# Performance work log

Measured on AMD Instinct MI355X. Metric: run time of the kernel, lower is better.

## Reference

```python
import jax, jax.numpy as jnp
import numpy as np

N_NODES = 100000
N_EDGES = 1600000
IN_DIM, HID_DIM, OUT_DIM = 128, 64, 40


def setup_inputs() -> dict:
    key = jax.random.key(0)
    k1, k2, k3, k4, k5, k6 = jax.random.split(key, 6)
    x = jax.random.normal(k1, (N_NODES, IN_DIM), dtype=jnp.float32)
    edge_index = jax.random.randint(k2, (2, N_EDGES), 0, N_NODES, dtype=jnp.int64)
    W1 = jax.random.normal(k3, (IN_DIM, HID_DIM), dtype=jnp.float32) * 0.05
    b1 = jnp.zeros((HID_DIM,), dtype=jnp.float32)
    W2 = jax.random.normal(k4, (HID_DIM, OUT_DIM), dtype=jnp.float32) * 0.05
    b2 = jnp.zeros((OUT_DIM,), dtype=jnp.float32)
    return {"x": x, "edge_index": edge_index, "W1": W1, "b1": b1, "W2": W2, "b2": b2}


def gcn_conv(x, src, dst, W, b, n_nodes):
    """PyG GCNConv: linear -> symmetric-normalized aggregation (with self loops) -> + bias."""
    h = x @ W                                                # [N, C_out]
    # degree of targets, including the implicit self loop (weight 1 each)
    deg = jax.ops.segment_sum(jnp.ones_like(dst, dtype=h.dtype), dst,
                              num_segments=n_nodes) + 1.0    # [N]
    dinv = jax.lax.rsqrt(deg)                                # deg >= 1, always valid
    norm = dinv[src] * dinv[dst]                             # [E] edge norm coefficients
    msg = h[src] * norm[:, None]                             # [E, C_out] gather + scale
    agg = jax.ops.segment_sum(msg, dst, num_segments=n_nodes)
    # self-loop contribution: norm_ii = dinv_i * dinv_i
    agg = agg + h * (dinv * dinv)[:, None]
    return agg + b


def reference(x, edge_index, W1, b1, W2, b2):
    src, dst = edge_index[0], edge_index[1]  # source_to_target flow (PyG default)
    n = x.shape[0]
    h = gcn_conv(x, src, dst, W1, b1, n)
    h = jax.nn.relu(h)
    # dropout is identity in eval mode (training=False)
    out = gcn_conv(h, src, dst, W2, b2, n)
    return out
```

## Files before the change

kernel.cpp:

```cpp
#include <hip/hip_runtime.h>
#include <math.h>

#define N_NODES 100000
#define N_EDGES 1600000
#define IN_DIM 128
#define HID_DIM 64
#define OUT_DIM 40

#define NPAD 102400

#define BUCKET_SHIFT 7
#define BUCKET_NODES 128
#define N_BUCKETS 782
#define CHUNK 2048
#define N_CHUNKS 784

typedef _Float16 f16;
typedef _Float16 f16x2 __attribute__((ext_vector_type(2)));
typedef _Float16 f16x4 __attribute__((ext_vector_type(4)));
typedef _Float16 f16x8 __attribute__((ext_vector_type(8)));
typedef float f32x4 __attribute__((ext_vector_type(4)));


__global__ __launch_bounds__(256) void hist_kernel(const int* __restrict__ dst,
                                                   int* __restrict__ hist) {
    __shared__ int lh[N_BUCKETS];
    int c = blockIdx.x;
    int t = threadIdx.x;
    for (int b = t; b < N_BUCKETS; b += 256) lh[b] = 0;
    __syncthreads();
    int e0 = c * CHUNK;
    for (int i = t; i < CHUNK; i += 256) {
        int e = e0 + i;
        if (e < N_EDGES) atomicAdd(&lh[dst[e] >> BUCKET_SHIFT], 1);
    }
    __syncthreads();
    for (int b = t; b < N_BUCKETS; b += 256) hist[c * N_BUCKETS + b] = lh[b];
}

__global__ __launch_bounds__(256) void scan_chunks_kernel(const int* __restrict__ hist,
                                                          int* __restrict__ base,
                                                          int* __restrict__ bucketTotal) {
    __shared__ int lds[256];
    int b = blockIdx.x;
    int t = threadIdx.x;
    int v[4];
    int s = 0;
    for (int k = 0; k < 4; ++k) {
        int c = 4 * t + k;
        int cv = (c < N_CHUNKS) ? hist[c * N_BUCKETS + b] : 0;
        v[k] = s;
        s += cv;
    }
    lds[t] = s;
    __syncthreads();
    for (int off = 1; off < 256; off <<= 1) {
        int val = (t >= off) ? lds[t - off] : 0;
        __syncthreads();
        lds[t] += val;
        __syncthreads();
    }
    int excl = (t == 0) ? 0 : lds[t - 1];
    for (int k = 0; k < 4; ++k) {
        int c = 4 * t + k;
        if (c < N_CHUNKS) base[b * N_CHUNKS + c] = excl + v[k];
    }
    if (t == 255) bucketTotal[b] = lds[255];
}

__global__ __launch_bounds__(256) void scan_buckets_kernel(const int* __restrict__ bucketTotal,
                                                           int* __restrict__ bucketBase) {
    __shared__ int lds[256];
    int t = threadIdx.x;
    int v[4];
    int s = 0;
    for (int k = 0; k < 4; ++k) {
        int b = 4 * t + k;
        int cv = (b < N_BUCKETS) ? bucketTotal[b] : 0;
        v[k] = s;
        s += cv;
    }
    lds[t] = s;
    __syncthreads();
    for (int off = 1; off < 256; off <<= 1) {
        int val = (t >= off) ? lds[t - off] : 0;
        __syncthreads();
        lds[t] += val;
        __syncthreads();
    }
    int excl = (t == 0) ? 0 : lds[t - 1];
    for (int k = 0; k < 4; ++k) {
        int b = 4 * t + k;
        if (b < N_BUCKETS) bucketBase[b] = excl + v[k];
    }
}

__global__ __launch_bounds__(256) void scatter_kernel(const int* __restrict__ src,
                                                      const int* __restrict__ dst,
                                                      const int* __restrict__ base,
                                                      const int* __restrict__ bucketBase,
                                                      int* __restrict__ stage) {
    __shared__ int lbase[N_BUCKETS];
    __shared__ int lcnt[N_BUCKETS];
    int bid = blockIdx.x;
    int chunk = (bid & 7) * 98 + (bid >> 3);
    int t = threadIdx.x;
    for (int b = t; b < N_BUCKETS; b += 256) {
        lbase[b] = base[b * N_CHUNKS + chunk] + bucketBase[b];
        lcnt[b] = 0;
    }
    __syncthreads();
    int e0 = chunk * CHUNK;
    for (int i = t; i < CHUNK; i += 256) {
        int e = e0 + i;
        if (e < N_EDGES) {
            int d = dst[e];
            int b = d >> BUCKET_SHIFT;
            int pos = lbase[b] + atomicAdd(&lcnt[b], 1);
            stage[pos] = ((d & (BUCKET_NODES - 1)) << 17) | src[e];
        }
    }
}

__global__ __launch_bounds__(256) void place_kernel(const int* __restrict__ stage,
                                                    const int* __restrict__ bucketBase,
                                                    int* __restrict__ csr,
                                                    int* __restrict__ row_start,
                                                    int* __restrict__ cnt,
                                                    float* __restrict__ dinv) {
    __shared__ int lhist[BUCKET_NODES];
    __shared__ int lscan[BUCKET_NODES];
    __shared__ int lstart[BUCKET_NODES];
    __shared__ int lcur[BUCKET_NODES];
    int b = blockIdx.x;
    int t = threadIdx.x;
    int est = bucketBase[b];
    int een = (b == N_BUCKETS - 1) ? N_EDGES : bucketBase[b + 1];
    if (t < BUCKET_NODES) { lhist[t] = 0; lcur[t] = 0; }
    __syncthreads();
    for (int e = est + t; e < een; e += 256) atomicAdd(&lhist[stage[e] >> 17], 1);
    __syncthreads();
    if (t < BUCKET_NODES) lscan[t] = lhist[t];
    __syncthreads();
    for (int off = 1; off < BUCKET_NODES; off <<= 1) {
        int val = (t >= off && t < BUCKET_NODES) ? lscan[t - off] : 0;
        __syncthreads();
        if (t < BUCKET_NODES) lscan[t] += val;
        __syncthreads();
    }
    if (t < BUCKET_NODES) {
        int myexcl = (t == 0) ? 0 : lscan[t - 1];
        lstart[t] = est + myexcl;
        int node = (b << BUCKET_SHIFT) + t;
        if (node < N_NODES) {
            row_start[node] = est + myexcl;
            cnt[node] = lhist[t];
            dinv[node] = rsqrtf((float)lhist[t] + 1.0f);
        }
    }
    __syncthreads();
    for (int e = est + t; e < een; e += 256) {
        int rec = stage[e];
        int dl = rec >> 17;
        int pos = lstart[dl] + atomicAdd(&lcur[dl], 1);
        csr[pos] = rec & 0x1FFFF;
    }
}

__global__ __launch_bounds__(256) void wfrag_kernel(const float* __restrict__ W1,
                                                    const float* __restrict__ W2,
                                                    f16* __restrict__ w1f,
                                                    f16* __restrict__ w2f) {
    int g = blockIdx.x * 256 + threadIdx.x;
    if (g < 1024) {
        int f = g >> 6, L = g & 63;
        int s = f >> 2, c = f & 3;
        int q = L >> 4, n = L & 15;
        f16x8 v;
#pragma unroll
        for (int j = 0; j < 8; ++j) v[j] = (f16)W1[(32 * s + 8 * q + j) * HID_DIM + 16 * c + n];
        *(f16x8*)&w1f[(size_t)g * 8] = v;
    } else if (g < 1024 + 384) {
        int gg = g - 1024;
        int f = gg >> 6, L = gg & 63;
        int s = f / 3, c = f % 3;
        int q = L >> 4, n = L & 15;
        int col = 16 * c + n;
        f16x8 v;
#pragma unroll
        for (int j = 0; j < 8; ++j)
            v[j] = (col < OUT_DIM) ? (f16)W2[(32 * s + 8 * q + j) * OUT_DIM + col] : (f16)0.f;
        *(f16x8*)&w2f[(size_t)gg * 8] = v;
    }
}

__global__ __launch_bounds__(256) void gemm1_kernel(const float* __restrict__ x,
                                                    const f16* __restrict__ w1f,
                                                    const float* __restrict__ dinv,
                                                    f16* __restrict__ h1p) {
    __shared__ f16 aT[1088 * 8];
    int t = threadIdx.x;
    int nodeBase = blockIdx.x * 64;
    int L = t & 63;

    const f16x8* w1f8 = (const f16x8*)w1f;
    f16x8 bfrag[16];
#pragma unroll
    for (int f = 0; f < 16; ++f) bfrag[f] = w1f8[f * 64 + L];

#pragma unroll
    for (int i = 0; i < 8; ++i) {
        int idx = i * 256 + t;
        int node = idx >> 5;
        int col4 = idx & 31;
        int gnode = nodeBase + node;
        if (gnode >= N_NODES) gnode = N_NODES - 1;
        float4 v = *(const float4*)&x[(size_t)gnode * IN_DIM + col4 * 4];
        int w = node >> 4, m = node & 15;
        int s = col4 >> 3, q = (col4 >> 1) & 3, j0 = (col4 & 1) * 4;
        f16x4 h;
        h.x = (f16)v.x; h.y = (f16)v.y; h.z = (f16)v.z; h.w = (f16)v.w;
        int idx16 = (w * 4 + s) * 68 + 17 * q + m;
        *(f16x4*)&aT[idx16 * 8 + j0] = h;
    }
    __syncthreads();

    int wv = t >> 6;
    int q = L >> 4, m = L & 15;
    f32x4 acc[4] = {};
#pragma unroll
    for (int s = 0; s < 4; ++s) {
        f16x8 afrag = *(const f16x8*)&aT[((wv * 4 + s) * 68 + 17 * q + m) * 8];
#pragma unroll
        for (int c = 0; c < 4; ++c)
            acc[c] = __builtin_amdgcn_mfma_f32_16x16x32_f16(afrag, bfrag[s * 4 + c], acc[c], 0, 0, 0);
    }

#pragma unroll
    for (int r = 0; r < 4; ++r) {
        int node = nodeBase + 16 * wv + q * 4 + r;
        if (node < N_NODES) {
            float di = dinv[node];
#pragma unroll
            for (int c = 0; c < 4; ++c)
                h1p[(size_t)node * HID_DIM + 16 * c + m] = (f16)(acc[c][r] * di);
        }
    }
}

#define ZSTR 72
__global__ __launch_bounds__(256) void agg1mm_kernel(const f16* __restrict__ h1p,
                                                     const int* __restrict__ csr,
                                                     const int* __restrict__ row_start,
                                                     const int* __restrict__ cnt,
                                                     const float* __restrict__ dinv,
                                                     const float* __restrict__ b1,
                                                     const f16* __restrict__ w2f,
                                                     f16* __restrict__ h2p) {
    __shared__ f16 zT[64 * ZSTR];
    int t = threadIdx.x;
    int nodeBase = blockIdx.x * 64;
    int wv = t >> 6;
    int L = t & 63;
    int g = L >> 3;
    int s = L & 7;
    const f16x8* h8 = (const f16x8*)h1p;
    float bb[8];
#pragma unroll
    for (int j = 0; j < 8; ++j) bb[j] = b1[8 * s + j];

    for (int p = 0; p < 2; ++p) {
        int nodeLocal = 16 * wv + 8 * p + g;
        int node = nodeBase + nodeLocal;
        float acc[8];
#pragma unroll
        for (int j = 0; j < 8; ++j) acc[j] = 0.f;
        int lim = 0;
        const int* cp = csr;
        bool valid = (node < N_NODES);
        if (valid) {
            f16x8 sv = h8[(size_t)node * 8 + s];
#pragma unroll
            for (int j = 0; j < 8; ++j) acc[j] = (float)sv[j];
            lim = cnt[node];
            cp = csr + row_start[node];
        }
        for (int k = 0; k < lim; k += 4) {
            int k1 = (k + 1 < lim) ? k + 1 : k;
            int k2 = (k + 2 < lim) ? k + 2 : k;
            int k3 = (k + 3 < lim) ? k + 3 : k;
            int i0 = cp[k], i1 = cp[k1], i2 = cp[k2], i3 = cp[k3];
            f16x8 f0 = h8[(size_t)i0 * 8 + s];
            f16x8 f1 = h8[(size_t)i1 * 8 + s];
            f16x8 f2 = h8[(size_t)i2 * 8 + s];
            f16x8 f3 = h8[(size_t)i3 * 8 + s];
            float m1 = (k + 1 < lim) ? 1.f : 0.f;
            float m2 = (k + 2 < lim) ? 1.f : 0.f;
            float m3 = (k + 3 < lim) ? 1.f : 0.f;
#pragma unroll
            for (int j = 0; j < 8; ++j)
                acc[j] += (float)f0[j] + m1 * (float)f1[j] + m2 * (float)f2[j] + m3 * (float)f3[j];
        }
        f16x8 o;
        if (valid) {
            float di = dinv[node];
#pragma unroll
            for (int j = 0; j < 8; ++j) {
                float v = acc[j] * di + bb[j];
                o[j] = (f16)(v > 0.f ? v : 0.f);
            }
        } else {
#pragma unroll
            for (int j = 0; j < 8; ++j) o[j] = (f16)0.f;
        }
        *(f16x8*)&zT[nodeLocal * ZSTR + 8 * s] = o;
    }
    __syncthreads();

    int q = L >> 4, m = L & 15;
    const f16x8* w2f8 = (const f16x8*)w2f;
    f32x4 acc2[3] = {};
#pragma unroll
    for (int ks = 0; ks < 2; ++ks) {
        f16x8 afrag = *(const f16x8*)&zT[(16 * wv + m) * ZSTR + 32 * ks + 8 * q];
#pragma unroll
        for (int c = 0; c < 3; ++c)
            acc2[c] = __builtin_amdgcn_mfma_f32_16x16x32_f16(afrag, w2f8[(ks * 3 + c) * 64 + L], acc2[c], 0, 0, 0);
    }
#pragma unroll
    for (int r = 0; r < 4; ++r) {
        int node = nodeBase + 16 * wv + q * 4 + r;
        if (node < N_NODES) {
            float di = dinv[node];
            h2p[(size_t)node * OUT_DIM + m]      = (f16)(acc2[0][r] * di);
            h2p[(size_t)node * OUT_DIM + 16 + m] = (f16)(acc2[1][r] * di);
            if (m < 8)
                h2p[(size_t)node * OUT_DIM + 32 + m] = (f16)(acc2[2][r] * di);
        }
    }
}

__global__ __launch_bounds__(256) void agg2_kernel(const f16* __restrict__ h2p,
                                                   const int* __restrict__ csr,
                                                   const int* __restrict__ row_start,
                                                   const int* __restrict__ cnt,
                                                   const float* __restrict__ dinv,
                                                   const float* __restrict__ b2,
                                                   float* __restrict__ out) {
    int t = threadIdx.x;
    int node = blockIdx.x * 32 + (t >> 3);
    int s = t & 7;
    if (node >= N_NODES || s >= 5) return;
    const f16x8* h8 = (const f16x8*)h2p;
    float acc[8];
    {
        f16x8 sv = h8[(size_t)node * 5 + s];
#pragma unroll
        for (int j = 0; j < 8; ++j) acc[j] = (float)sv[j];
    }
    int lim = cnt[node];
    const int* cp = csr + row_start[node];
    for (int k = 0; k < lim; k += 4) {
        int k1 = (k + 1 < lim) ? k + 1 : k;
        int k2 = (k + 2 < lim) ? k + 2 : k;
        int k3 = (k + 3 < lim) ? k + 3 : k;
        int i0 = cp[k], i1 = cp[k1], i2 = cp[k2], i3 = cp[k3];
        f16x8 f0 = h8[(size_t)i0 * 5 + s];
        f16x8 f1 = h8[(size_t)i1 * 5 + s];
        f16x8 f2 = h8[(size_t)i2 * 5 + s];
        f16x8 f3 = h8[(size_t)i3 * 5 + s];
        float m1 = (k + 1 < lim) ? 1.f : 0.f;
        float m2 = (k + 2 < lim) ? 1.f : 0.f;
        float m3 = (k + 3 < lim) ? 1.f : 0.f;
#pragma unroll
        for (int j = 0; j < 8; ++j)
            acc[j] += (float)f0[j] + m1 * (float)f1[j] + m2 * (float)f2[j] + m3 * (float)f3[j];
    }
    float di = dinv[node];
    float4 o0, o1;
    o0.x = acc[0] * di + b2[8 * s + 0];
    o0.y = acc[1] * di + b2[8 * s + 1];
    o0.z = acc[2] * di + b2[8 * s + 2];
    o0.w = acc[3] * di + b2[8 * s + 3];
    o1.x = acc[4] * di + b2[8 * s + 4];
    o1.y = acc[5] * di + b2[8 * s + 5];
    o1.z = acc[6] * di + b2[8 * s + 6];
    o1.w = acc[7] * di + b2[8 * s + 7];
    *(float4*)&out[(size_t)node * OUT_DIM + 8 * s] = o0;
    *(float4*)&out[(size_t)node * OUT_DIM + 8 * s + 4] = o1;
}

extern "C" void kernel_launch(void* const* d_in, const int* in_sizes, int n_in,
                              void* d_out, int out_size, void* d_ws, size_t ws_size,
                              hipStream_t stream) {
    const float* x  = (const float*)d_in[0];
    const int*   ei = (const int*)d_in[1];
    const float* W1 = (const float*)d_in[2];
    const float* b1 = (const float*)d_in[3];
    const float* W2 = (const float*)d_in[4];
    const float* b2 = (const float*)d_in[5];
    float* out = (float*)d_out;

    const int* src = ei;
    const int* dst = ei + N_EDGES;

    int* wsi        = (int*)d_ws;
    int* hist       = wsi;
    int* base       = hist + N_CHUNKS * N_BUCKETS;
    int* bucketTotal= base + N_BUCKETS * N_CHUNKS;
    int* bucketBase = bucketTotal + 1024;
    int* row_start  = bucketBase + 1024;
    int* cnt        = row_start + NPAD;
    int* csr        = cnt + NPAD;
    int* stage      = csr + N_EDGES;
    float* dinv     = (float*)(stage + N_EDGES);
    f16*   h1p      = (f16*)(dinv + NPAD);
    f16*   h2p      = h1p + (size_t)N_NODES * HID_DIM;
    f16*   w1f      = h2p + (size_t)N_NODES * OUT_DIM;
    f16*   w2f      = w1f + 8192;

    hist_kernel<<<N_CHUNKS, 256, 0, stream>>>(dst, hist);
    scan_chunks_kernel<<<N_BUCKETS, 256, 0, stream>>>(hist, base, bucketTotal);
    scan_buckets_kernel<<<1, 256, 0, stream>>>(bucketTotal, bucketBase);
    scatter_kernel<<<N_CHUNKS, 256, 0, stream>>>(src, dst, base, bucketBase, stage);
    place_kernel<<<N_BUCKETS, 256, 0, stream>>>(stage, bucketBase, csr, row_start, cnt, dinv);

    wfrag_kernel<<<6, 256, 0, stream>>>(W1, W2, w1f, w2f);
    gemm1_kernel<<<(N_NODES + 63) / 64, 256, 0, stream>>>(x, w1f, dinv, h1p);
    agg1mm_kernel<<<(N_NODES + 63) / 64, 256, 0, stream>>>(h1p, csr, row_start, cnt, dinv, b1, w2f, h2p);
    agg2_kernel<<<(N_NODES + 31) / 32, 256, 0, stream>>>(h2p, csr, row_start, cnt, dinv, b2, out);
}
```

Before: 217.3 us.

## Fuse all GCN stages into one persistent cooperative kernel with grid syncs

Replaces the nine separate launches (histogram, scans, scatter, place, weight fragmenting, gemm1, agg1+mm, agg2) with a single cooperative persistent kernel. Each stage loops over its work items with a grid-stride loop and the stages are separated by grid.sync(). This targets per-launch overhead and inter-kernel gaps. In exchange it adds grid-wide barrier cost, caps occupancy at the cooperative grid size, and forces all stages to share one register and shared-memory footprint.

```diff
diff --git a/kernel.cpp b/kernel.cpp
--- a/kernel.cpp
+++ b/kernel.cpp
@@ -1,5 +1,8 @@
 #include <hip/hip_runtime.h>
+#include <hip/hip_cooperative_groups.h>
 #include <math.h>
+
+namespace cg = cooperative_groups;
 
 #define N_NODES 100000
 #define N_EDGES 1600000
@@ -15,379 +18,394 @@
 #define CHUNK 2048
 #define N_CHUNKS 784
 
+#define G1_TILES 1563
+#define AGG2_TILES 3125
+
 typedef _Float16 f16;
 typedef _Float16 f16x2 __attribute__((ext_vector_type(2)));
 typedef _Float16 f16x4 __attribute__((ext_vector_type(4)));
 typedef _Float16 f16x8 __attribute__((ext_vector_type(8)));
 typedef float f32x4 __attribute__((ext_vector_type(4)));
 
-
-__global__ __launch_bounds__(256) void hist_kernel(const int* __restrict__ dst,
-                                                   int* __restrict__ hist) {
-    __shared__ int lh[N_BUCKETS];
-    int c = blockIdx.x;
+#define ZSTR 72
+
+__global__ __launch_bounds__(256) void gcn_mega_kernel(
+    const float* __restrict__ x, const int* __restrict__ ei,
+    const float* __restrict__ W1, const float* __restrict__ b1,
+    const float* __restrict__ W2, const float* __restrict__ b2,
+    float* __restrict__ out, int* __restrict__ wsi)
+{
+    int* hist        = wsi;
+    int* base        = hist + N_CHUNKS * N_BUCKETS;
+    int* bucketTotal = base + N_BUCKETS * N_CHUNKS;
+    int* bucketBase  = bucketTotal + 1024;
+    int* row_start   = bucketBase + 1024;
+    int* cnt         = row_start + NPAD;
+    int* csr         = cnt + NPAD;
+    int* stage       = csr + N_EDGES;
+    float* dinv      = (float*)(stage + N_EDGES);
+    f16* h1p         = (f16*)(dinv + NPAD);
+    f16* h2p         = h1p + (size_t)N_NODES * HID_DIM;
+    f16* w1f         = h2p + (size_t)N_NODES * OUT_DIM;
+    f16* w2f         = w1f + 8192;
+    const int* src = ei;
+    const int* dst = ei + N_EDGES;
+
+    cg::grid_group grid = cg::this_grid();
+    __shared__ alignas(16) unsigned char smemraw[17408];
     int t = threadIdx.x;
-    for (int b = t; b < N_BUCKETS; b += 256) lh[b] = 0;
-    __syncthreads();
-    int e0 = c * CHUNK;
-    for (int i = t; i < CHUNK; i += 256) {
-        int e = e0 + i;
-        if (e < N_EDGES) atomicAdd(&lh[dst[e] >> BUCKET_SHIFT], 1);
-    }
-    __syncthreads();
-    for (int b = t; b < N_BUCKETS; b += 256) hist[c * N_BUCKETS + b] = lh[b];
-}
-
-__global__ __launch_bounds__(256) void scan_chunks_kernel(const int* __restrict__ hist,
-                                                          int* __restrict__ base,
-                                                          int* __restrict__ bucketTotal) {
-    __shared__ int lds[256];
-    int b = blockIdx.x;
-    int t = threadIdx.x;
-    int v[4];
-    int s = 0;
-    for (int k = 0; k < 4; ++k) {
-        int c = 4 * t + k;
-        int cv = (c < N_CHUNKS) ? hist[c * N_BUCKETS + b] : 0;
-        v[k] = s;
-        s += cv;
-    }
-    lds[t] = s;
-    __syncthreads();
-    for (int off = 1; off < 256; off <<= 1) {
-        int val = (t >= off) ? lds[t - off] : 0;
+    int G = gridDim.x;
+
+    {
+        int* lh = (int*)smemraw;
+        for (int c = blockIdx.x; c < N_CHUNKS; c += G) {
+            for (int b = t; b < N_BUCKETS; b += 256) lh[b] = 0;
+            __syncthreads();
+            int e0 = c * CHUNK;
+            for (int i = t; i < CHUNK; i += 256) {
+                int e = e0 + i;
+                if (e < N_EDGES) atomicAdd(&lh[dst[e] >> BUCKET_SHIFT], 1);
+            }
+            __syncthreads();
+            for (int b = t; b < N_BUCKETS; b += 256) hist[c * N_BUCKETS + b] = lh[b];
+            __syncthreads();
+        }
+    }
+    grid.sync();
+
+    {
+        int* lds = (int*)smemraw;
+        for (int b = blockIdx.x; b < N_BUCKETS; b += G) {
+            int v[4];
+            int s = 0;
+            for (int k = 0; k < 4; ++k) {
+                int c = 4 * t + k;
+                int cv = (c < N_CHUNKS) ? hist[c * N_BUCKETS + b] : 0;
+                v[k] = s;
+                s += cv;
+            }
+            lds[t] = s;
+            __syncthreads();
+            for (int off = 1; off < 256; off <<= 1) {
+                int val = (t >= off) ? lds[t - off] : 0;
+                __syncthreads();
+                lds[t] += val;
+                __syncthreads();
+            }
+            int excl = (t == 0) ? 0 : lds[t - 1];
+            for (int k = 0; k < 4; ++k) {
+                int c = 4 * t + k;
+                if (c < N_CHUNKS) base[b * N_CHUNKS + c] = excl + v[k];
+            }
+            if (t == 255) bucketTotal[b] = lds[255];
+            __syncthreads();
+        }
+    }
+    grid.sync();
+
+    if (blockIdx.x == 0) {
+        int* lds = (int*)smemraw;
+        int v[4];
+        int s = 0;
+        for (int k = 0; k < 4; ++k) {
+            int b = 4 * t + k;
+            int cv = (b < N_BUCKETS) ? bucketTotal[b] : 0;
+            v[k] = s;
+            s += cv;
+        }
+        lds[t] = s;
         __syncthreads();
-        lds[t] += val;
-        __syncthreads();
-    }
-    int excl = (t == 0) ? 0 : lds[t - 1];
-    for (int k = 0; k < 4; ++k) {
-        int c = 4 * t + k;
-        if (c < N_CHUNKS) base[b * N_CHUNKS + c] = excl + v[k];
-    }
-    if (t == 255) bucketTotal[b] = lds[255];
-}
-
-__global__ __launch_bounds__(256) void scan_buckets_kernel(const int* __restrict__ bucketTotal,
-                                                           int* __restrict__ bucketBase) {
-    __shared__ int lds[256];
-    int t = threadIdx.x;
-    int v[4];
-    int s = 0;
-    for (int k = 0; k < 4; ++k) {
-        int b = 4 * t + k;
-        int cv = (b < N_BUCKETS) ? bucketTotal[b] : 0;
-        v[k] = s;
-        s += cv;
-    }
-    lds[t] = s;
-    __syncthreads();
-    for (int off = 1; off < 256; off <<= 1) {
-        int val = (t >= off) ? lds[t - off] : 0;
-        __syncthreads();
-        lds[t] += val;
-        __syncthreads();
-    }
-    int excl = (t == 0) ? 0 : lds[t - 1];
-    for (int k = 0; k < 4; ++k) {
-        int b = 4 * t + k;
-        if (b < N_BUCKETS) bucketBase[b] = excl + v[k];
-    }
-}
-
-__global__ __launch_bounds__(256) void scatter_kernel(const int* __restrict__ src,
-                                                      const int* __restrict__ dst,
-                                                      const int* __restrict__ base,
-                                                      const int* __restrict__ bucketBase,
-                                                      int* __restrict__ stage) {
-    __shared__ int lbase[N_BUCKETS];
-    __shared__ int lcnt[N_BUCKETS];
-    int bid = blockIdx.x;
-    int chunk = (bid & 7) * 98 + (bid >> 3);
-    int t = threadIdx.x;
-    for (int b = t; b < N_BUCKETS; b += 256) {
-        lbase[b] = base[b * N_CHUNKS + chunk] + bucketBase[b];
-        lcnt[b] = 0;
-    }
-    __syncthreads();
-    int e0 = chunk * CHUNK;
-    for (int i = t; i < CHUNK; i += 256) {
-        int e = e0 + i;
-        if (e < N_EDGES) {
-            int d = dst[e];
-            int b = d >> BUCKET_SHIFT;
-            int pos = lbase[b] + atomicAdd(&lcnt[b], 1);
-            stage[pos] = ((d & (BUCKET_NODES - 1)) << 17) | src[e];
-        }
-    }
-}
-
-__global__ __launch_bounds__(256) void place_kernel(const int* __restrict__ stage,
-                                                    const int* __restrict__ bucketBase,
-                                                    int* __restrict__ csr,
-                                                    int* __restrict__ row_start,
-                                                    int* __restrict__ cnt,
-                                                    float* __restrict__ dinv) {
-    __shared__ int lhist[BUCKET_NODES];
-    __shared__ int lscan[BUCKET_NODES];
-    __shared__ int lstart[BUCKET_NODES];
-    __shared__ int lcur[BUCKET_NODES];
-    int b = blockIdx.x;
-    int t = threadIdx.x;
-    int est = bucketBase[b];
-    int een = (b == N_BUCKETS - 1) ? N_EDGES : bucketBase[b + 1];
-    if (t < BUCKET_NODES) { lhist[t] = 0; lcur[t] = 0; }
-    __syncthreads();
-    for (int e = est + t; e < een; e += 256) atomicAdd(&lhist[stage[e] >> 17], 1);
-    __syncthreads();
-    if (t < BUCKET_NODES) lscan[t] = lhist[t];
-    __syncthreads();
-    for (int off = 1; off < BUCKET_NODES; off <<= 1) {
-        int val = (t >= off && t < BUCKET_NODES) ? lscan[t - off] : 0;
-        __syncthreads();
-        if (t < BUCKET_NODES) lscan[t] += val;
-        __syncthreads();
-    }
-    if (t < BUCKET_NODES) {
-        int myexcl = (t == 0) ? 0 : lscan[t - 1];
-        lstart[t] = est + myexcl;
-        int node = (b << BUCKET_SHIFT) + t;
-        if (node < N_NODES) {
-            row_start[node] = est + myexcl;
-            cnt[node] = lhist[t];
-            dinv[node] = rsqrtf((float)lhist[t] + 1.0f);
-        }
-    }
-    __syncthreads();
-    for (int e = est + t; e < een; e += 256) {
-        int rec = stage[e];
-        int dl = rec >> 17;
-        int pos = lstart[dl] + atomicAdd(&lcur[dl], 1);
-        csr[pos] = rec & 0x1FFFF;
-    }
-}
-
-__global__ __launch_bounds__(256) void wfrag_kernel(const float* __restrict__ W1,
-                                                    const float* __restrict__ W2,
-                                                    f16* __restrict__ w1f,
-                                                    f16* __restrict__ w2f) {
-    int g = blockIdx.x * 256 + threadIdx.x;
-    if (g < 1024) {
-        int f = g >> 6, L = g & 63;
-        int s = f >> 2, c = f & 3;
-        int q = L >> 4, n = L & 15;
-        f16x8 v;
-#pragma unroll
-        for (int j = 0; j < 8; ++j) v[j] = (f16)W1[(32 * s + 8 * q + j) * HID_DIM + 16 * c + n];
-        *(f16x8*)&w1f[(size_t)g * 8] = v;
-    } else if (g < 1024 + 384) {
-        int gg = g - 1024;
-        int f = gg >> 6, L = gg & 63;
-        int s = f / 3, c = f % 3;
-        int q = L >> 4, n = L & 15;
-        int col = 16 * c + n;
-        f16x8 v;
-#pragma unroll
-        for (int j = 0; j < 8; ++j)
-            v[j] = (col < OUT_DIM) ? (f16)W2[(32 * s + 8 * q + j) * OUT_DIM + col] : (f16)0.f;
-        *(f16x8*)&w2f[(size_t)gg * 8] = v;
-    }
-}
-
-__global__ __launch_bounds__(256) void gemm1_kernel(const float* __restrict__ x,
-                                                    const f16* __restrict__ w1f,
-                                                    const float* __restrict__ dinv,
-                                                    f16* __restrict__ h1p) {
-    __shared__ f16 aT[1088 * 8];
-    int t = threadIdx.x;
-    int nodeBase = blockIdx.x * 64;
-    int L = t & 63;
-
-    const f16x8* w1f8 = (const f16x8*)w1f;
-    f16x8 bfrag[16];
-#pragma unroll
-    for (int f = 0; f < 16; ++f) bfrag[f] = w1f8[f * 64 + L];
-
-#pragma unroll
-    for (int i = 0; i < 8; ++i) {
-        int idx = i * 256 + t;
-        int node = idx >> 5;
-        int col4 = idx & 31;
-        int gnode = nodeBase + node;
-        if (gnode >= N_NODES) gnode = N_NODES - 1;
-        float4 v = *(const float4*)&x[(size_t)gnode * IN_DIM + col4 * 4];
-        int w = node >> 4, m = node & 15;
-        int s = col4 >> 3, q = (col4 >> 1) & 3, j0 = (col4 & 1) * 4;
-        f16x4 h;
-        h.x = (f16)v.x; h.y = (f16)v.y; h.z = (f16)v.z; h.w = (f16)v.w;
-        int idx16 = (w * 4 + s) * 68 + 17 * q + m;
-        *(f16x4*)&aT[idx16 * 8 + j0] = h;
-    }
-    __syncthreads();
-
-    int wv = t >> 6;
-    int q = L >> 4, m = L & 15;
-    f32x4 acc[4] = {};
-#pragma unroll
-    for (int s = 0; s < 4; ++s) {
-        f16x8 afrag = *(const f16x8*)&aT[((wv * 4 + s) * 68 + 17 * q + m) * 8];
-#pragma unroll
-        for (int c = 0; c < 4; ++c)
-            acc[c] = __builtin_amdgcn_mfma_f32_16x16x32_f16(afrag, bfrag[s * 4 + c], acc[c], 0, 0, 0);
-    }
-
-#pragma unroll
-    for (int r = 0; r < 4; ++r) {
-        int node = nodeBase + 16 * wv + q * 4 + r;
-        if (node < N_NODES) {
-            float di = dinv[node];
-#pragma unroll
-            for (int c = 0; c < 4; ++c)
-                h1p[(size_t)node * HID_DIM + 16 * c + m] = (f16)(acc[c][r] * di);
-        }
-    }
-}
-
-#define ZSTR 72
-__global__ __launch_bounds__(256) void agg1mm_kernel(const f16* __restrict__ h1p,
-                                                     const int* __restrict__ csr,
-                                                     const int* __restrict__ row_start,
-                                                     const int* __restrict__ cnt,
-                                                     const float* __restrict__ dinv,
-                                                     const float* __restrict__ b1,
-                                                     const f16* __restrict__ w2f,
-                                                     f16* __restrict__ h2p) {
-    __shared__ f16 zT[64 * ZSTR];
-    int t = threadIdx.x;
-    int nodeBase = blockIdx.x * 64;
-    int wv = t >> 6;
-    int L = t & 63;
-    int g = L >> 3;
-    int s = L & 7;
-    const f16x8* h8 = (const f16x8*)h1p;
-    float bb[8];
-#pragma unroll
-    for (int j = 0; j < 8; ++j) bb[j] = b1[8 * s + j];
-
-    for (int p = 0; p < 2; ++p) {
-        int nodeLocal = 16 * wv + 8 * p + g;
-        int node = nodeBase + nodeLocal;
-        float acc[8];
-#pragma unroll
-        for (int j = 0; j < 8; ++j) acc[j] = 0.f;
-        int lim = 0;
-        const int* cp = csr;
-        bool valid = (node < N_NODES);
-        if (valid) {
-            f16x8 sv = h8[(size_t)node * 8 + s];
-#pragma unroll
-            for (int j = 0; j < 8; ++j) acc[j] = (float)sv[j];
-            lim = cnt[node];
-            cp = csr + row_start[node];
-        }
-        for (int k = 0; k < lim; k += 4) {
-            int k1 = (k + 1 < lim) ? k + 1 : k;
-            int k2 = (k + 2 < lim) ? k + 2 : k;
-            int k3 = (k + 3 < lim) ? k + 3 : k;
-            int i0 = cp[k], i1 = cp[k1], i2 = cp[k2], i3 = cp[k3];
-            f16x8 f0 = h8[(size_t)i0 * 8 + s];
-            f16x8 f1 = h8[(size_t)i1 * 8 + s];
-            f16x8 f2 = h8[(size_t)i2 * 8 + s];
-            f16x8 f3 = h8[(size_t)i3 * 8 + s];
-            float m1 = (k + 1 < lim) ? 1.f : 0.f;
-            float m2 = (k + 2 < lim) ? 1.f : 0.f;
-            float m3 = (k + 3 < lim) ? 1.f : 0.f;
-#pragma unroll
-            for (int j = 0; j < 8; ++j)
-                acc[j] += (float)f0[j] + m1 * (float)f1[j] + m2 * (float)f2[j] + m3 * (float)f3[j];
-        }
-        f16x8 o;
-        if (valid) {
-            float di = dinv[node];
-#pragma unroll
-            for (int j = 0; j < 8; ++j) {
-                float v = acc[j] * di + bb[j];
-                o[j] = (f16)(v > 0.f ? v : 0.f);
-            }
-        } else {
-#pragma unroll
-            for (int j = 0; j < 8; ++j) o[j] = (f16)0.f;
-        }
-        *(f16x8*)&zT[nodeLocal * ZSTR + 8 * s] = o;
-    }
-    __syncthreads();
-
-    int q = L >> 4, m = L & 15;
-    const f16x8* w2f8 = (const f16x8*)w2f;
-    f32x4 acc2[3] = {};
-#pragma unroll
-    for (int ks = 0; ks < 2; ++ks) {
-        f16x8 afrag = *(const f16x8*)&zT[(16 * wv + m) * ZSTR + 32 * ks + 8 * q];
-#pragma unroll
-        for (int c = 0; c < 3; ++c)
-            acc2[c] = __builtin_amdgcn_mfma_f32_16x16x32_f16(afrag, w2f8[(ks * 3 + c) * 64 + L], acc2[c], 0, 0, 0);
-    }
-#pragma unroll
-    for (int r = 0; r < 4; ++r) {
-        int node = nodeBase + 16 * wv + q * 4 + r;
-        if (node < N_NODES) {
-            float di = dinv[node];
-            h2p[(size_t)node * OUT_DIM + m]      = (f16)(acc2[0][r] * di);
-            h2p[(size_t)node * OUT_DIM + 16 + m] = (f16)(acc2[1][r] * di);
-            if (m < 8)
-                h2p[(size_t)node * OUT_DIM + 32 + m] = (f16)(acc2[2][r] * di);
-        }
-    }
-}
-
-__global__ __launch_bounds__(256) void agg2_kernel(const f16* __restrict__ h2p,
-                                                   const int* __restrict__ csr,
-                                                   const int* __restrict__ row_start,
-                                                   const int* __restrict__ cnt,
-                                                   const float* __restrict__ dinv,
-                                                   const float* __restrict__ b2,
-                                                   float* __restrict__ out) {
-    int t = threadIdx.x;
-    int node = blockIdx.x * 32 + (t >> 3);
-    int s = t & 7;
-    if (node >= N_NODES || s >= 5) return;
-    const f16x8* h8 = (const f16x8*)h2p;
-    float acc[8];
-    {
-        f16x8 sv = h8[(size_t)node * 5 + s];
-#pragma unroll
-        for (int j = 0; j < 8; ++j) acc[j] = (float)sv[j];
-    }
-    int lim = cnt[node];
-    const int* cp = csr + row_start[node];
-    for (int k = 0; k < lim; k += 4) {
-        int k1 = (k + 1 < lim) ? k + 1 : k;
-        int k2 = (k + 2 < lim) ? k + 2 : k;
-        int k3 = (k + 3 < lim) ? k + 3 : k;
-        int i0 = cp[k], i1 = cp[k1], i2 = cp[k2], i3 = cp[k3];
-        f16x8 f0 = h8[(size_t)i0 * 5 + s];
-        f16x8 f1 = h8[(size_t)i1 * 5 + s];
-        f16x8 f2 = h8[(size_t)i2 * 5 + s];
-        f16x8 f3 = h8[(size_t)i3 * 5 + s];
-        float m1 = (k + 1 < lim) ? 1.f : 0.f;
-        float m2 = (k + 2 < lim) ? 1.f : 0.f;
-        float m3 = (k + 3 < lim) ? 1.f : 0.f;
-#pragma unroll
-        for (int j = 0; j < 8; ++j)
-            acc[j] += (float)f0[j] + m1 * (float)f1[j] + m2 * (float)f2[j] + m3 * (float)f3[j];
-    }
-    float di = dinv[node];
-    float4 o0, o1;
-    o0.x = acc[0] * di + b2[8 * s + 0];
-    o0.y = acc[1] * di + b2[8 * s + 1];
-    o0.z = acc[2] * di + b2[8 * s + 2];
-    o0.w = acc[3] * di + b2[8 * s + 3];
-    o1.x = acc[4] * di + b2[8 * s + 4];
-    o1.y = acc[5] * di + b2[8 * s + 5];
-    o1.z = acc[6] * di + b2[8 * s + 6];
-    o1.w = acc[7] * di + b2[8 * s + 7];
-    *(float4*)&out[(size_t)node * OUT_DIM + 8 * s] = o0;
-    *(float4*)&out[(size_t)node * OUT_DIM + 8 * s + 4] = o1;
+        for (int off = 1; off < 256; off <<= 1) {
+            int val = (t >= off) ? lds[t - off] : 0;
+            __syncthreads();
+            lds[t] += val;
+            __syncthreads();
+        }
+        int excl = (t == 0) ? 0 : lds[t - 1];
+        for (int k = 0; k < 4; ++k) {
+            int b = 4 * t + k;
+            if (b < N_BUCKETS) bucketBase[b] = excl + v[k];
+        }
+    }
+    grid.sync();
+
+    {
+        int* lbase = (int*)smemraw;
+        int* lcnt  = lbase + N_BUCKETS;
+        for (int job = blockIdx.x; job < N_CHUNKS; job += G) {
+            int chunk = (job & 7) * 98 + (job >> 3);
+            for (int b = t; b < N_BUCKETS; b += 256) {
+                lbase[b] = base[b * N_CHUNKS + chunk] + bucketBase[b];
+                lcnt[b] = 0;
+            }
+            __syncthreads();
+            int e0 = chunk * CHUNK;
+            for (int i = t; i < CHUNK; i += 256) {
+                int e = e0 + i;
+                if (e < N_EDGES) {
+                    int d = dst[e];
+                    int b = d >> BUCKET_SHIFT;
+                    int pos = lbase[b] + atomicAdd(&lcnt[b], 1);
+                    stage[pos] = ((d & (BUCKET_NODES - 1)) << 17) | src[e];
+                }
+            }
+            __syncthreads();
+        }
+    }
+    grid.sync();
+
+    {
+        int* lhist  = (int*)smemraw;
+        int* lscan  = lhist + BUCKET_NODES;
+        int* lstart = lscan + BUCKET_NODES;
+        int* lcur   = lstart + BUCKET_NODES;
+        for (int job = blockIdx.x; job < N_BUCKETS + 2; job += G) {
+            if (job < N_BUCKETS) {
+                int b = job;
+                int est = bucketBase[b];
+                int een = (b == N_BUCKETS - 1) ? N_EDGES : bucketBase[b + 1];
+                if (t < BUCKET_NODES) { lhist[t] = 0; lcur[t] = 0; }
+                __syncthreads();
+                for (int e = est + t; e < een; e += 256) atomicAdd(&lhist[stage[e] >> 17], 1);
+                __syncthreads();
+                if (t < BUCKET_NODES) lscan[t] = lhist[t];
+                __syncthreads();
+                for (int off = 1; off < BUCKET_NODES; off <<= 1) {
+                    int val = (t >= off && t < BUCKET_NODES) ? lscan[t - off] : 0;
+                    __syncthreads();
+                    if (t < BUCKET_NODES) lscan[t] += val;
+                    __syncthreads();
+                }
+                if (t < BUCKET_NODES) {
+                    int myexcl = (t == 0) ? 0 : lscan[t - 1];
+                    lstart[t] = est + myexcl;
+                    int node = (b << BUCKET_SHIFT) + t;
+                    if (node < N_NODES) {
+                        row_start[node] = est + myexcl;
+                        cnt[node] = lhist[t];
+                        dinv[node] = rsqrtf((float)lhist[t] + 1.0f);
+                    }
+                }
+                __syncthreads();
+                for (int e = est + t; e < een; e += 256) {
+                    int rec = stage[e];
+                    int dl = rec >> 17;
+                    int pos = lstart[dl] + atomicAdd(&lcur[dl], 1);
+                    csr[pos] = rec & 0x1FFFF;
+                }
+                __syncthreads();
+            } else if (job == N_BUCKETS) {
+                for (int g2 = t; g2 < 1024; g2 += 256) {
+                    int f = g2 >> 6, L = g2 & 63;
+                    int s = f >> 2, c = f & 3;
+                    int q = L >> 4, n = L & 15;
+                    f16x8 v;
+#pragma unroll
+                    for (int j = 0; j < 8; ++j)
+                        v[j] = (f16)W1[(32 * s + 8 * q + j) * HID_DIM + 16 * c + n];
+                    *(f16x8*)&w1f[(size_t)g2 * 8] = v;
+                }
+            } else {
+                for (int g2 = t; g2 < 384; g2 += 256) {
+                    int f = g2 >> 6, L = g2 & 63;
+                    int s = f / 3, c = f % 3;
+                    int q = L >> 4, n = L & 15;
+                    int col = 16 * c + n;
+                    f16x8 v;
+#pragma unroll
+                    for (int j = 0; j < 8; ++j)
+                        v[j] = (col < OUT_DIM) ? (f16)W2[(32 * s + 8 * q + j) * OUT_DIM + col] : (f16)0.f;
+                    *(f16x8*)&w2f[(size_t)g2 * 8] = v;
+                }
+            }
+        }
+    }
+    grid.sync();
+
+    {
+        f16* aT = (f16*)smemraw;
+        int L = t & 63;
+        const f16x8* w1f8 = (const f16x8*)w1f;
+        f16x8 bfrag[16];
+#pragma unroll
+        for (int f = 0; f < 16; ++f) bfrag[f] = w1f8[f * 64 + L];
+
+        for (int job = blockIdx.x; job < G1_TILES; job += G) {
+            int nodeBase = job * 64;
+#pragma unroll
+            for (int i = 0; i < 8; ++i) {
+                int idx = i * 256 + t;
+                int node = idx >> 5;
+                int col4 = idx & 31;
+                int gnode = nodeBase + node;
+                if (gnode >= N_NODES) gnode = N_NODES - 1;
+                float4 v = *(const float4*)&x[(size_t)gnode * IN_DIM + col4 * 4];
+                int w = node >> 4, m = node & 15;
+                int s = col4 >> 3, q = (col4 >> 1) & 3, j0 = (col4 & 1) * 4;
+                f16x4 h;
+                h.x = (f16)v.x; h.y = (f16)v.y; h.z = (f16)v.z; h.w = (f16)v.w;
+                int idx16 = (w * 4 + s) * 68 + 17 * q + m;
+                *(f16x4*)&aT[idx16 * 8 + j0] = h;
+            }
+            __syncthreads();
+
+            int wv = t >> 6;
+            int q = L >> 4, m = L & 15;
+            f32x4 acc[4] = {};
+#pragma unroll
+            for (int s = 0; s < 4; ++s) {
+                f16x8 afrag = *(const f16x8*)&aT[((wv * 4 + s) * 68 + 17 * q + m) * 8];
+#pragma unroll
+                for (int c = 0; c < 4; ++c)
+                    acc[c] = __builtin_amdgcn_mfma_f32_16x16x32_f16(afrag, bfrag[s * 4 + c], acc[c], 0, 0, 0);
+            }
+#pragma unroll
+            for (int r = 0; r < 4; ++r) {
+                int node = nodeBase + 16 * wv + q * 4 + r;
+                if (node < N_NODES) {
+                    float di = dinv[node];
+#pragma unroll
+                    for (int c = 0; c < 4; ++c)
+                        h1p[(size_t)node * HID_DIM + 16 * c + m] = (f16)(acc[c][r] * di);
+                }
+            }
+            __syncthreads();
+        }
+    }
+    grid.sync();
+
+    {
+        f16* zT = (f16*)smemraw;
+        int wv = t >> 6;
+        int L = t & 63;
+        int g = L >> 3;
+        int s = L & 7;
+        const f16x8* h8 = (const f16x8*)h1p;
+        float bb[8];
+#pragma unroll
+        for (int j = 0; j < 8; ++j) bb[j] = b1[8 * s + j];
+        const f16x8* w2f8 = (const f16x8*)w2f;
+
+        for (int job = blockIdx.x; job < G1_TILES; job += G) {
+            int nodeBase = job * 64;
+            for (int p = 0; p < 2; ++p) {
+                int nodeLocal = 16 * wv + 8 * p + g;
+                int node = nodeBase + nodeLocal;
+                float acc[8];
+#pragma unroll
+                for (int j = 0; j < 8; ++j) acc[j] = 0.f;
+                int lim = 0;
+                const int* cp = csr;
+                bool valid = (node < N_NODES);
+                if (valid) {
+                    f16x8 sv = h8[(size_t)node * 8 + s];
+#pragma unroll
+                    for (int j = 0; j < 8; ++j) acc[j] = (float)sv[j];
+                    lim = cnt[node];
+                    cp = csr + row_start[node];
+                }
+                for (int k = 0; k < lim; k += 4) {
+                    int k1 = (k + 1 < lim) ? k + 1 : k;
+                    int k2 = (k + 2 < lim) ? k + 2 : k;
+                    int k3 = (k + 3 < lim) ? k + 3 : k;
+                    int i0 = cp[k], i1 = cp[k1], i2 = cp[k2], i3 = cp[k3];
+                    f16x8 f0 = h8[(size_t)i0 * 8 + s];
+                    f16x8 f1 = h8[(size_t)i1 * 8 + s];
+                    f16x8 f2 = h8[(size_t)i2 * 8 + s];
+                    f16x8 f3 = h8[(size_t)i3 * 8 + s];
+                    float m1 = (k + 1 < lim) ? 1.f : 0.f;
+                    float m2 = (k + 2 < lim) ? 1.f : 0.f;
+                    float m3 = (k + 3 < lim) ? 1.f : 0.f;
+#pragma unroll
+                    for (int j = 0; j < 8; ++j)
+                        acc[j] += (float)f0[j] + m1 * (float)f1[j] + m2 * (float)f2[j] + m3 * (float)f3[j];
+                }
+                f16x8 o;
+                if (valid) {
+                    float di = dinv[node];
+#pragma unroll
+                    for (int j = 0; j < 8; ++j) {
+                        float v = acc[j] * di + bb[j];
+                        o[j] = (f16)(v > 0.f ? v : 0.f);
+                    }
+                } else {
+#pragma unroll
+                    for (int j = 0; j < 8; ++j) o[j] = (f16)0.f;
+                }
+                *(f16x8*)&zT[nodeLocal * ZSTR + 8 * s] = o;
+            }
+            __syncthreads();
+
+            int q = L >> 4, m = L & 15;
+            f32x4 acc2[3] = {};
+#pragma unroll
+            for (int ks = 0; ks < 2; ++ks) {
+                f16x8 afrag = *(const f16x8*)&zT[(16 * wv + m) * ZSTR + 32 * ks + 8 * q];
+#pragma unroll
+                for (int c = 0; c < 3; ++c)
+                    acc2[c] = __builtin_amdgcn_mfma_f32_16x16x32_f16(afrag, w2f8[(ks * 3 + c) * 64 + L], acc2[c], 0, 0, 0);
+            }
+#pragma unroll
+            for (int r = 0; r < 4; ++r) {
+                int node = nodeBase + 16 * wv + q * 4 + r;
+                if (node < N_NODES) {
+                    float di = dinv[node];
+                    h2p[(size_t)node * OUT_DIM + m]      = (f16)(acc2[0][r] * di);
+                    h2p[(size_t)node * OUT_DIM + 16 + m] = (f16)(acc2[1][r] * di);
+                    if (m < 8)
+                        h2p[(size_t)node * OUT_DIM + 32 + m] = (f16)(acc2[2][r] * di);
+                }
+            }
+            __syncthreads();
+        }
+    }
+    grid.sync();
+
+    {
+        int s = t & 7;
+        const f16x8* h8 = (const f16x8*)h2p;
+        for (int job = blockIdx.x; job < AGG2_TILES; job += G) {
+            int node = job * 32 + (t >> 3);
+            if (node < N_NODES && s < 5) {
+                float acc[8];
+                {
+                    f16x8 sv = h8[(size_t)node * 5 + s];
+#pragma unroll
+                    for (int j = 0; j < 8; ++j) acc[j] = (float)sv[j];
+                }
+                int lim = cnt[node];
+                const int* cp = csr + row_start[node];
+                for (int k = 0; k < lim; k += 4) {
+                    int k1 = (k + 1 < lim) ? k + 1 : k;
+                    int k2 = (k + 2 < lim) ? k + 2 : k;
+                    int k3 = (k + 3 < lim) ? k + 3 : k;
+                    int i0 = cp[k], i1 = cp[k1], i2 = cp[k2], i3 = cp[k3];
+                    f16x8 f0 = h8[(size_t)i0 * 5 + s];
+                    f16x8 f1 = h8[(size_t)i1 * 5 + s];
+                    f16x8 f2 = h8[(size_t)i2 * 5 + s];
+                    f16x8 f3 = h8[(size_t)i3 * 5 + s];
+                    float m1 = (k + 1 < lim) ? 1.f : 0.f;
+                    float m2 = (k + 2 < lim) ? 1.f : 0.f;
+                    float m3 = (k + 3 < lim) ? 1.f : 0.f;
+#pragma unroll
+                    for (int j = 0; j < 8; ++j)
+                        acc[j] += (float)f0[j] + m1 * (float)f1[j] + m2 * (float)f2[j] + m3 * (float)f3[j];
+                }
+                float di = dinv[node];
+                float4 o0, o1;
+                o0.x = acc[0] * di + b2[8 * s + 0];
+                o0.y = acc[1] * di + b2[8 * s + 1];
+                o0.z = acc[2] * di + b2[8 * s + 2];
+                o0.w = acc[3] * di + b2[8 * s + 3];
+                o1.x = acc[4] * di + b2[8 * s + 4];
+                o1.y = acc[5] * di + b2[8 * s + 5];
+                o1.z = acc[6] * di + b2[8 * s + 6];
+                o1.w = acc[7] * di + b2[8 * s + 7];
+                *(float4*)&out[(size_t)node * OUT_DIM + 8 * s] = o0;
+                *(float4*)&out[(size_t)node * OUT_DIM + 8 * s + 4] = o1;
+            }
+        }
+    }
 }
 
 extern "C" void kernel_launch(void* const* d_in, const int* in_sizes, int n_in,
@@ -399,34 +417,16 @@
     const float* b1 = (const float*)d_in[3];
     const float* W2 = (const float*)d_in[4];
     const float* b2 = (const float*)d_in[5];
-    float* out = (float*)d_out;
-
-    const int* src = ei;
-    const int* dst = ei + N_EDGES;
-
-    int* wsi        = (int*)d_ws;
-    int* hist       = wsi;
-    int* base       = hist + N_CHUNKS * N_BUCKETS;
-    int* bucketTotal= base + N_BUCKETS * N_CHUNKS;
-    int* bucketBase = bucketTotal + 1024;
-    int* row_start  = bucketBase + 1024;
-    int* cnt        = row_start + NPAD;
-    int* csr        = cnt + NPAD;
-    int* stage      = csr + N_EDGES;
-    float* dinv     = (float*)(stage + N_EDGES);
-    f16*   h1p      = (f16*)(dinv + NPAD);
-    f16*   h2p      = h1p + (size_t)N_NODES * HID_DIM;
-    f16*   w1f      = h2p + (size_t)N_NODES * OUT_DIM;
-    f16*   w2f      = w1f + 8192;
-
-    hist_kernel<<<N_CHUNKS, 256, 0, stream>>>(dst, hist);
-    scan_chunks_kernel<<<N_BUCKETS, 256, 0, stream>>>(hist, base, bucketTotal);
-    scan_buckets_kernel<<<1, 256, 0, stream>>>(bucketTotal, bucketBase);
-    scatter_kernel<<<N_CHUNKS, 256, 0, stream>>>(src, dst, base, bucketBase, stage);
-    place_kernel<<<N_BUCKETS, 256, 0, stream>>>(stage, bucketBase, csr, row_start, cnt, dinv);
-
-    wfrag_kernel<<<6, 256, 0, stream>>>(W1, W2, w1f, w2f);
-    gemm1_kernel<<<(N_NODES + 63) / 64, 256, 0, stream>>>(x, w1f, dinv, h1p);
-    agg1mm_kernel<<<(N_NODES + 63) / 64, 256, 0, stream>>>(h1p, csr, row_start, cnt, dinv, b1, w2f, h2p);
-    agg2_kernel<<<(N_NODES + 31) / 32, 256, 0, stream>>>(h2p, csr, row_start, cnt, dinv, b2, out);
+    float* outp = (float*)d_out;
+    int* wsi = (int*)d_ws;
+
+    int maxb = 0;
+    hipOccupancyMaxActiveBlocksPerMultiprocessor(&maxb, gcn_mega_kernel, 256, 0);
+    if (maxb < 1) maxb = 1;
+    if (maxb > 8) maxb = 8;
+    int grid = maxb * 256;
+
+    void* args[] = {(void*)&x, (void*)&ei, (void*)&W1, (void*)&b1,
+                    (void*)&W2, (void*)&b2, (void*)&outp, (void*)&wsi};
+    hipLaunchCooperativeKernel(gcn_mega_kernel, dim3(grid), dim3(256), args, 0, stream);
 }
```

Result: slower. 548.2 us (+152.3%).
